# Optimization experiments

Hardware: AMD Instinct MI355X
Metric: run time of the kernel (lower is better)

## Reference

```python
import jax, jax.numpy as jnp
import numpy as np
import jax.scipy.linalg

BATCH = 1048576
M_NUM = 2
DT = 0.0166667
NN_RATIO = 0.5
SLOPE = 0.01  # torch LeakyReLU default negative_slope


def setup_inputs() -> dict:
    key = jax.random.key(0)
    ks = jax.random.split(key, 16)
    inp = {}
    inp["SS"] = jax.random.normal(ks[0], (BATCH, 2), dtype=jnp.float32)
    inp["Alphas"] = jax.random.uniform(ks[1], (BATCH, M_NUM), dtype=jnp.float32)
    # per-muscle scalar parameters (positive so sqrt(K*I) is valid)
    inp["K0s"] = jax.random.uniform(ks[2], (M_NUM,), minval=0.5, maxval=1.5)
    inp["K1s"] = jax.random.uniform(ks[3], (M_NUM,), minval=0.5, maxval=1.5)
    inp["L0s"] = jax.random.uniform(ks[4], (M_NUM,), minval=0.5, maxval=1.5)
    inp["L1s"] = jax.random.uniform(ks[5], (M_NUM,), minval=0.1, maxval=0.6)
    inp["Ms"] = jnp.array([1.0, -1.0], dtype=jnp.float32)  # moment arms
    inp["I_p"] = jnp.array([1.0], dtype=jnp.float32)
    inp["B_p"] = jnp.array([0.05], dtype=jnp.float32)
    inp["K_p"] = jnp.array([1.0], dtype=jnp.float32)
    # per-muscle compensational MLP weights: 3-32-32-32-1 (eval mode, dropout off)
    s = 0.1
    inp["W1"] = jax.random.normal(ks[6], (M_NUM, 3, 32)) * s
    inp["b1"] = jax.random.normal(ks[7], (M_NUM, 32)) * s
    inp["W2"] = jax.random.normal(ks[8], (M_NUM, 32, 32)) * s
    inp["b2"] = jax.random.normal(ks[9], (M_NUM, 32)) * s
    inp["W3"] = jax.random.normal(ks[10], (M_NUM, 32, 32)) * s
    inp["b3"] = jax.random.normal(ks[11], (M_NUM, 32)) * s
    inp["W4"] = jax.random.normal(ks[12], (M_NUM, 32, 1)) * s
    inp["b4"] = jax.random.normal(ks[13], (M_NUM, 1)) * s
    return inp


def _leaky(x):
    return jnp.where(x >= 0, x, SLOPE * x)


def reference(SS, Alphas, K0s, K1s, L0s, L1s, Ms, I_p, B_p, K_p,
              W1, b1, W2, b2, W3, b3, W4, b4):
    B = SS.shape[0]
    a = jnp.clip(Alphas, 0.0, 1.0)                      # (B, m)
    # muscle length / speed via scalar moment arms
    l = SS[:, 0:1] * Ms[None, :]                        # (B, m)
    dl = SS[:, 1:2] * Ms[None, :]                       # (B, m)
    # compensational MLPs, vectorized over muscles
    x = jnp.stack([l, dl, a], axis=-1)                  # (B, m, 3)
    h = _leaky(jnp.einsum('bmi,mio->bmo', x, W1) + b1[None])
    h = _leaky(jnp.einsum('bmi,mio->bmo', h, W2) + b2[None])
    h = _leaky(jnp.einsum('bmi,mio->bmo', h, W3) + b3[None])
    nn_out = jnp.tanh(jnp.einsum('bmi,mio->bmo', h, W4) + b4[None])[..., 0] * NN_RATIO  # (B, m)

    I0, B0p, K0p = I_p[0], B_p[0], K_p[0]
    K_m = K0s[None, :] + K1s[None, :] * a               # (B, m)
    K_tot = jnp.sum(K_m * Ms[None, :] ** 2, axis=1)     # (B,)
    A10 = -(K_tot + K0p) / I0
    D = 2.0 * jnp.sqrt(K_tot * I0)
    A11 = -(D + B0p) / I0
    B_F = K_m * (L0s[None, :] + L1s[None, :] * a - jnp.abs(l)) \
        + K1s[None, :] * L1s[None, :] * a * a * nn_out   # (B, m)
    B10 = jnp.sum(B_F * Ms[None, :], axis=1) / I0       # (B,)

    # Build block matrix M6 = [[A*dt, B*dt, 0], [0, 0, I2], [0, 0, 0]]
    M6 = jnp.zeros((B, 6, 6), dtype=SS.dtype)
    M6 = M6.at[:, 0, 1].set(DT)
    M6 = M6.at[:, 1, 0].set(A10 * DT)
    M6 = M6.at[:, 1, 1].set(A11 * DT)
    M6 = M6.at[:, 1, 2].set(B10 * DT)
    M6 = M6.at[:, 1, 3].set(DT / I0)
    M6 = M6.at[:, 2, 4].set(1.0)
    M6 = M6.at[:, 3, 5].set(1.0)

    expMT = jax.vmap(jax.scipy.linalg.expm)(M6)         # (B, 6, 6)
    Ad = expMT[:, :2, :2]
    Bd1 = expMT[:, :2, 4:6]
    Bd0 = expMT[:, :2, 2:4] - Bd1
    u = jnp.array([1.0, 0.0], dtype=SS.dtype)           # U0 = U1 = [1, 0]
    SSout = (jnp.einsum('bij,bj->bi', Ad, SS)
             + jnp.einsum('bij,j->bi', Bd0, u)
             + jnp.einsum('bij,j->bi', Bd1, u))          # (B, 2)
    return SSout[:, :1], SSout
```

## Files before the change

kernel.cpp:

```cpp
#include <hip/hip_runtime.h>
#include <hip/hip_bf16.h>

#define NTHREADS 256
#define WAVES    4
#define GPW      4
#define DT_F     0.0166667f

typedef _Float16 f16x4 __attribute__((ext_vector_type(4)));
typedef _Float16 f16x2 __attribute__((ext_vector_type(2)));
typedef float    f32x4 __attribute__((ext_vector_type(4)));

#define BF16_PROBE 0xBF803F80u

#define OW1 0
#define OB1 192
#define OW2 256
#define OB2 2304
#define OW3 2368
#define OB3 4416
#define OW4 4480
#define OB4 4544
#define SMEM_F 4560

__device__ __forceinline__ float leaky(float x) { return fmaxf(x, 0.01f * x); }

__device__ __forceinline__ float tanh_fast(float x) {
    const float xc = fminf(fmaxf(x, -10.0f), 10.0f);
    const float t  = __expf(2.0f * xc);
    return (t - 1.0f) * __builtin_amdgcn_rcpf(t + 1.0f);
}

__device__ __forceinline__ f16x2 pkrtz(float a, float b) {
    return __builtin_bit_cast(f16x2, __builtin_amdgcn_cvt_pkrtz(a, b));
}

__device__ __forceinline__ f16x4 leaky_cvt(const f32x4 D) {
    f16x2 lo = pkrtz(D[0], D[1]);
    f16x2 hi = pkrtz(D[2], D[3]);
    const f16x2 sl = {(_Float16)0.01f, (_Float16)0.01f};
    lo = __builtin_elementwise_max(lo, lo * sl);
    hi = __builtin_elementwise_max(hi, hi * sl);
    return __builtin_shufflevector(lo, hi, 0, 1, 2, 3);
}

__device__ __forceinline__ void epilogue_math(
    const float* P, float ss0, float ss1, float a0, float a1,
    float nn0, float nn1, float& o0f, float& o1f)
{
    const float K00 = P[0], K01 = P[1], K10 = P[2], K11 = P[3];
    const float L00 = P[4], L01 = P[5], L10 = P[6], L11 = P[7];
    const float Ms0 = P[8], Ms1 = P[9];
    const float I0  = P[10], B0p = P[11], K0p = P[12];

    const float Km0   = fmaf(K10, a0, K00);
    const float Km1   = fmaf(K11, a1, K01);
    const float K_tot = Km0*Ms0*Ms0 + Km1*Ms1*Ms1;
    const float invI  = 1.0f / I0;
    const float A10   = -(K_tot + K0p) * invI;
    const float Dd    = 2.0f * sqrtf(K_tot * I0);
    const float A11   = -(Dd + B0p) * invI;
    const float absl0 = fabsf(ss0 * Ms0);
    const float absl1 = fabsf(ss0 * Ms1);
    const float BF0   = Km0 * (L00 + L10*a0 - absl0) + K10*L10*a0*a0*nn0;
    const float BF1   = Km1 * (L01 + L11*a1 - absl1) + K11*L11*a1*a1*nn1;
    const float B10   = (BF0*Ms0 + BF1*Ms1) * invI;

    const float t01 = DT_F;
    const float t10 = A10 * DT_F;
    const float t11 = A11 * DT_F;

    float p00 = 1.0f/5040.0f, p01 = 0.0f, p10 = 0.0f, p11 = 1.0f/5040.0f;
    const float coef[6] = {1.0f/720.0f, 1.0f/120.0f, 1.0f/24.0f,
                           1.0f/6.0f,   0.5f,        1.0f};
    #pragma unroll
    for (int j = 0; j < 6; ++j) {
        const float cj  = coef[j];
        const float n00 = p01*t10 + cj;
        const float n01 = p00*t01 + p01*t11;
        const float n10 = p11*t10;
        const float n11 = p10*t01 + p11*t11 + cj;
        p00 = n00; p01 = n01; p10 = n10; p11 = n11;
    }
    const float e00 = 1.0f + t01*p10;
    const float e01 = t01*p11;
    const float e10 = t10*p00 + t11*p10;
    const float e11 = 1.0f + t10*p01 + t11*p11;

    const float cscale = DT_F * B10;
    o0f = fmaf(e00, ss0, fmaf(e01, ss1, p01 * cscale));
    o1f = fmaf(e10, ss0, fmaf(e11, ss1, p11 * cscale));
}

__device__ __forceinline__ float ldb(const __hip_bfloat16* p, int i) {
    return __bfloat162float(p[i]);
}

__device__ void run_bf16_fallback(
    const void* SSv, const void* ALv, const void* K0sv, const void* K1sv,
    const void* L0sv, const void* L1sv, const void* Msv, const void* I_pv,
    const void* B_pv, const void* K_pv, const void* W1v, const void* b1v,
    const void* W2v, const void* b2v, const void* W3v, const void* b3v,
    const void* W4v, const void* b4v, void* outv, int batch)
{
    const __hip_bfloat16* SS = (const __hip_bfloat16*)SSv;
    const __hip_bfloat16* AL = (const __hip_bfloat16*)ALv;
    const __hip_bfloat16* W1 = (const __hip_bfloat16*)W1v;
    const __hip_bfloat16* b1 = (const __hip_bfloat16*)b1v;
    const __hip_bfloat16* W2 = (const __hip_bfloat16*)W2v;
    const __hip_bfloat16* b2 = (const __hip_bfloat16*)b2v;
    const __hip_bfloat16* W3 = (const __hip_bfloat16*)W3v;
    const __hip_bfloat16* b3 = (const __hip_bfloat16*)b3v;
    const __hip_bfloat16* W4 = (const __hip_bfloat16*)W4v;
    const __hip_bfloat16* b4 = (const __hip_bfloat16*)b4v;

    float P[13];
    P[0] = ldb((const __hip_bfloat16*)K0sv, 0); P[1] = ldb((const __hip_bfloat16*)K0sv, 1);
    P[2] = ldb((const __hip_bfloat16*)K1sv, 0); P[3] = ldb((const __hip_bfloat16*)K1sv, 1);
    P[4] = ldb((const __hip_bfloat16*)L0sv, 0); P[5] = ldb((const __hip_bfloat16*)L0sv, 1);
    P[6] = ldb((const __hip_bfloat16*)L1sv, 0); P[7] = ldb((const __hip_bfloat16*)L1sv, 1);
    P[8] = ldb((const __hip_bfloat16*)Msv, 0);  P[9] = ldb((const __hip_bfloat16*)Msv, 1);
    P[10] = ldb((const __hip_bfloat16*)I_pv, 0);
    P[11] = ldb((const __hip_bfloat16*)B_pv, 0);
    P[12] = ldb((const __hip_bfloat16*)K_pv, 0);

    const int stride = gridDim.x * blockDim.x;
    for (int e = blockIdx.x * blockDim.x + threadIdx.x; e < batch; e += stride) {
        const float ss0 = ldb(SS, 2*e), ss1 = ldb(SS, 2*e+1);
        float a0 = fminf(fmaxf(ldb(AL, 2*e),   0.0f), 1.0f);
        float a1 = fminf(fmaxf(ldb(AL, 2*e+1), 0.0f), 1.0f);
        float nn[2];
        #pragma unroll 1
        for (int m = 0; m < 2; ++m) {
            const float am = m ? a1 : a0;
            const float l = ss0 * P[8+m], dl = ss1 * P[8+m];
            float h[32];
            #pragma unroll
            for (int o = 0; o < 32; ++o)
                h[o] = leaky(fmaf(l, ldb(W1, m*96+o),
                             fmaf(dl, ldb(W1, m*96+32+o),
                             fmaf(am, ldb(W1, m*96+64+o), ldb(b1, m*32+o)))));
            float g[32];
            #pragma unroll 1
            for (int oc = 0; oc < 4; ++oc) {
                float acc[8];
                #pragma unroll
                for (int j = 0; j < 8; ++j) acc[j] = ldb(b2, m*32+oc*8+j);
                #pragma unroll
                for (int k = 0; k < 32; ++k) {
                    #pragma unroll
                    for (int j = 0; j < 8; ++j)
                        acc[j] = fmaf(h[k], ldb(W2, m*1024+k*32+oc*8+j), acc[j]);
                }
                #pragma unroll
                for (int j = 0; j < 8; ++j) g[oc*8+j] = leaky(acc[j]);
            }
            float h3[32];
            #pragma unroll 1
            for (int oc = 0; oc < 4; ++oc) {
                float acc[8];
                #pragma unroll
                for (int j = 0; j < 8; ++j) acc[j] = ldb(b3, m*32+oc*8+j);
                #pragma unroll
                for (int k = 0; k < 32; ++k) {
                    #pragma unroll
                    for (int j = 0; j < 8; ++j)
                        acc[j] = fmaf(g[k], ldb(W3, m*1024+k*32+oc*8+j), acc[j]);
                }
                #pragma unroll
                for (int j = 0; j < 8; ++j) h3[oc*8+j] = leaky(acc[j]);
            }
            float acc = ldb(b4, m);
            #pragma unroll
            for (int k = 0; k < 32; ++k) acc = fmaf(h3[k], ldb(W4, m*32+k), acc);
            nn[m] = tanh_fast(acc) * 0.5f;
        }
        float o0f, o1f;
        epilogue_math(P, ss0, ss1, a0, a1, nn[0], nn[1], o0f, o1f);
        __hip_bfloat16* out0 = (__hip_bfloat16*)outv;
        __hip_bfloat162* out1 = (__hip_bfloat162*)(out0 + batch);
        out0[e] = __float2bfloat16(o0f);
        __hip_bfloat162 pr;
        pr.x = __float2bfloat16(o0f);
        pr.y = __float2bfloat16(o1f);
        out1[e] = pr;
    }
}

__global__ __launch_bounds__(NTHREADS) void joint_kernel(
    const void* __restrict__ SSv, const void* __restrict__ ALv,
    const void* __restrict__ K0sv, const void* __restrict__ K1sv,
    const void* __restrict__ L0sv, const void* __restrict__ L1sv,
    const void* __restrict__ Msv,  const void* __restrict__ I_pv,
    const void* __restrict__ B_pv, const void* __restrict__ K_pv,
    const void* __restrict__ W1v,  const void* __restrict__ b1v,
    const void* __restrict__ W2v,  const void* __restrict__ b2v,
    const void* __restrict__ W3v,  const void* __restrict__ b3v,
    const void* __restrict__ W4v,  const void* __restrict__ b4v,
    void* __restrict__ outv, int batch)
{
    const unsigned probe = *(const unsigned*)Msv;
    if (probe == BF16_PROBE) {
        run_bf16_fallback(SSv, ALv, K0sv, K1sv, L0sv, L1sv, Msv, I_pv, B_pv,
                          K_pv, W1v, b1v, W2v, b2v, W3v, b3v, W4v, b4v,
                          outv, batch);
        return;
    }

    const float* SS = (const float*)SSv;
    const float* AL = (const float*)ALv;
    const float* W1 = (const float*)W1v;  const float* b1 = (const float*)b1v;
    const float* W2 = (const float*)W2v;  const float* b2 = (const float*)b2v;
    const float* W3 = (const float*)W3v;  const float* b3 = (const float*)b3v;
    const float* W4 = (const float*)W4v;  const float* b4 = (const float*)b4v;

    const int tid  = threadIdx.x;
    const int wave = tid >> 6;
    const int lane = tid & 63;
    const int n    = lane & 15;
    const int q    = lane >> 4;

    __shared__ __align__(16) float sm[SMEM_F];
    for (int i = tid; i < 192;  i += NTHREADS) sm[OW1+i] = W1[i];
    for (int i = tid; i < 2048; i += NTHREADS) { sm[OW2+i] = W2[i]; sm[OW3+i] = W3[i]; }
    for (int i = tid; i < 64;   i += NTHREADS) {
        sm[OB1+i] = b1[i]; sm[OB2+i] = b2[i];
        sm[OB3+i] = b3[i]; sm[OW4+i] = W4[i];
    }
    if (tid < 2) sm[OB4+tid] = b4[tid];
    __syncthreads();

    f16x4 A1[2][2];
    #pragma unroll
    for (int mi = 0; mi < 2; ++mi)
        #pragma unroll
        for (int i = 0; i < 2; ++i)
            #pragma unroll
            for (int j = 0; j < 4; ++j) {
                const int k = q*4 + j;
                float v = 0.0f;
                if (k < 3)       v = sm[OW1 + mi*96 + k*32 + i*16 + n];
                else if (k == 3) v = sm[OB1 + mi*32 + i*16 + n];
                A1[mi][i][j] = (_Float16)v;
            }
    f16x4 A2[2][2][2], A3[2][2][2];
    #pragma unroll
    for (int mi = 0; mi < 2; ++mi)
        #pragma unroll
        for (int i = 0; i < 2; ++i)
            #pragma unroll
            for (int kb = 0; kb < 2; ++kb)
                #pragma unroll
                for (int j = 0; j < 4; ++j) {
                    const int in = kb*16 + q*4 + j;
                    A2[mi][i][kb][j] = (_Float16)sm[OW2 + mi*1024 + in*32 + i*16 + n];
                    A3[mi][i][kb][j] = (_Float16)sm[OW3 + mi*1024 + in*32 + i*16 + n];
                }
    f16x4 A4[2][2];
    #pragma unroll
    for (int mi = 0; mi < 2; ++mi)
        #pragma unroll
        for (int kb = 0; kb < 2; ++kb)
            #pragma unroll
            for (int j = 0; j < 4; ++j)
                A4[mi][kb][j] = (_Float16)sm[OW4 + mi*32 + kb*16 + q*4 + j];
    f32x4 Cb2[2][2], Cb3[2][2];
    #pragma unroll
    for (int mi = 0; mi < 2; ++mi) {
        #pragma unroll
        for (int i = 0; i < 2; ++i) {
            Cb2[mi][i] = *(const f32x4*)&sm[OB2 + mi*32 + i*16 + q*4];
            Cb3[mi][i] = *(const f32x4*)&sm[OB3 + mi*32 + i*16 + q*4];
        }
    }
    const float b4s0 = sm[OB4], b4s1 = sm[OB4+1];

    float P[13];
    P[0]  = ((const float*)K0sv)[0]; P[1]  = ((const float*)K0sv)[1];
    P[2]  = ((const float*)K1sv)[0]; P[3]  = ((const float*)K1sv)[1];
    P[4]  = ((const float*)L0sv)[0]; P[5]  = ((const float*)L0sv)[1];
    P[6]  = ((const float*)L1sv)[0]; P[7]  = ((const float*)L1sv)[1];
    P[8]  = ((const float*)Msv)[0];  P[9]  = ((const float*)Msv)[1];
    P[10] = ((const float*)I_pv)[0];
    P[11] = ((const float*)B_pv)[0];
    P[12] = ((const float*)K_pv)[0];

    const f32x4 zero = {0.0f, 0.0f, 0.0f, 0.0f};
    const int groupBase = (blockIdx.x * WAVES + wave) * GPW;

    #pragma unroll 1
    for (int g = 0; g < GPW; ++g) {
        const int ebase = (groupBase + g) * 64;
        float my_r0 = 0.0f, my_r1 = 0.0f;

        #pragma unroll 1
        for (int p = 0; p < 2; ++p) {
            const int t0 = 2*p, t1 = 2*p + 1;

            float2 s[2], al[2];
            float a0c[2], a1c[2];
            #pragma unroll
            for (int ti = 0; ti < 2; ++ti) {
                const int e  = ebase + (2*p + ti)*16 + n;
                const int eg = min(e, batch - 1);
                s[ti]  = ((const float2*)SS)[eg];
                al[ti] = ((const float2*)AL)[eg];
                a0c[ti] = fminf(fmaxf(al[ti].x, 0.0f), 1.0f);
                a1c[ti] = fminf(fmaxf(al[ti].y, 0.0f), 1.0f);
            }

            f16x4 B1[2][2];
            #pragma unroll
            for (int ti = 0; ti < 2; ++ti)
                #pragma unroll
                for (int mi = 0; mi < 2; ++mi) {
                    const float Msm = P[8 + mi];
                    const float am  = mi ? a1c[ti] : a0c[ti];
                    const f16x2 blo = pkrtz(s[ti].x * Msm, s[ti].y * Msm);
                    const f16x2 bhi = pkrtz(am, 1.0f);
                    B1[ti][mi] = __builtin_shufflevector(blo, bhi, 0, 1, 2, 3);
                }

            f32x4 D[2][2][2];
            #pragma unroll
            for (int ti = 0; ti < 2; ++ti)
                #pragma unroll
                for (int mi = 0; mi < 2; ++mi) {
                    D[ti][mi][0] = __builtin_amdgcn_mfma_f32_16x16x16f16(A1[mi][0], B1[ti][mi], zero, 0, 0, 0);
                    D[ti][mi][1] = __builtin_amdgcn_mfma_f32_16x16x16f16(A1[mi][1], B1[ti][mi], zero, 0, 0, 0);
                }
            f16x4 Bx[2][2][2];
            #pragma unroll
            for (int ti = 0; ti < 2; ++ti)
                #pragma unroll
                for (int mi = 0; mi < 2; ++mi) {
                    Bx[ti][mi][0] = leaky_cvt(D[ti][mi][0]);
                    Bx[ti][mi][1] = leaky_cvt(D[ti][mi][1]);
                }

            #pragma unroll
            for (int ti = 0; ti < 2; ++ti)
                #pragma unroll
                for (int mi = 0; mi < 2; ++mi) {
                    D[ti][mi][0] = __builtin_amdgcn_mfma_f32_16x16x16f16(A2[mi][0][1], Bx[ti][mi][1],
                                   __builtin_amdgcn_mfma_f32_16x16x16f16(A2[mi][0][0], Bx[ti][mi][0],
                                       Cb2[mi][0], 0, 0, 0), 0, 0, 0);
                    D[ti][mi][1] = __builtin_amdgcn_mfma_f32_16x16x16f16(A2[mi][1][1], Bx[ti][mi][1],
                                   __builtin_amdgcn_mfma_f32_16x16x16f16(A2[mi][1][0], Bx[ti][mi][0],
                                       Cb2[mi][1], 0, 0, 0), 0, 0, 0);
                }
            #pragma unroll
            for (int ti = 0; ti < 2; ++ti)
                #pragma unroll
                for (int mi = 0; mi < 2; ++mi) {
                    Bx[ti][mi][0] = leaky_cvt(D[ti][mi][0]);
                    Bx[ti][mi][1] = leaky_cvt(D[ti][mi][1]);
                }

            #pragma unroll
            for (int ti = 0; ti < 2; ++ti)
                #pragma unroll
                for (int mi = 0; mi < 2; ++mi) {
                    D[ti][mi][0] = __builtin_amdgcn_mfma_f32_16x16x16f16(A3[mi][0][1], Bx[ti][mi][1],
                                   __builtin_amdgcn_mfma_f32_16x16x16f16(A3[mi][0][0], Bx[ti][mi][0],
                                       Cb3[mi][0], 0, 0, 0), 0, 0, 0);
                    D[ti][mi][1] = __builtin_amdgcn_mfma_f32_16x16x16f16(A3[mi][1][1], Bx[ti][mi][1],
                                   __builtin_amdgcn_mfma_f32_16x16x16f16(A3[mi][1][0], Bx[ti][mi][0],
                                       Cb3[mi][1], 0, 0, 0), 0, 0, 0);
                }
            #pragma unroll
            for (int ti = 0; ti < 2; ++ti)
                #pragma unroll
                for (int mi = 0; mi < 2; ++mi) {
                    Bx[ti][mi][0] = leaky_cvt(D[ti][mi][0]);
                    Bx[ti][mi][1] = leaky_cvt(D[ti][mi][1]);
                }

            #pragma unroll
            for (int ti = 0; ti < 2; ++ti) {
                const bool own = (q == (2*p + ti));
                #pragma unroll
                for (int mi = 0; mi < 2; ++mi) {
                    f32x4 G = __builtin_amdgcn_mfma_f32_16x16x16f16(A4[mi][1], Bx[ti][mi][1],
                              __builtin_amdgcn_mfma_f32_16x16x16f16(A4[mi][0], Bx[ti][mi][0],
                                  zero, 0, 0, 0), 0, 0, 0);
                    const float r = G[0] + (mi ? b4s1 : b4s0);
                    if (mi == 0) my_r0 = own ? r : my_r0;
                    else         my_r1 = own ? r : my_r1;
                }
            }
        }

        const int eo  = ebase + lane;
        const int eog = min(eo, batch - 1);
        const float2 se  = ((const float2*)SS)[eog];
        const float2 ale = ((const float2*)AL)[eog];
        const float a0 = fminf(fmaxf(ale.x, 0.0f), 1.0f);
        const float a1 = fminf(fmaxf(ale.y, 0.0f), 1.0f);
        const float nn0 = tanh_fast(my_r0) * 0.5f;
        const float nn1 = tanh_fast(my_r1) * 0.5f;
        float o0f, o1f;
        epilogue_math(P, se.x, se.y, a0, a1, nn0, nn1, o0f, o1f);
        if (eo < batch) {
            ((float*)outv)[eo] = o0f;
            ((float2*)((float*)outv + batch))[eo] = make_float2(o0f, o1f);
        }
    }
}

extern "C" void kernel_launch(void* const* d_in, const int* in_sizes, int n_in,
                              void* d_out, int out_size, void* d_ws, size_t ws_size,
                              hipStream_t stream) {
    const int batch = in_sizes[0] / 2;
    const int elemsPerBlock = 64 * GPW * WAVES;
    const int grid = (batch + elemsPerBlock - 1) / elemsPerBlock;
    joint_kernel<<<grid, NTHREADS, 0, stream>>>(
        d_in[0], d_in[1], d_in[2], d_in[3], d_in[4], d_in[5], d_in[6],
        d_in[7], d_in[8], d_in[9], d_in[10], d_in[11], d_in[12], d_in[13],
        d_in[14], d_in[15], d_in[16], d_in[17], d_out, batch);
}
```

Baseline: 129.2 us.

## Use persistent grid-stride waves, pad weight LDS rows, shorten expm Taylor series

```diff
diff --git a/kernel.cpp b/kernel.cpp
--- a/kernel.cpp
+++ b/kernel.cpp
@@ -1,9 +1,9 @@
 #include <hip/hip_runtime.h>
 #include <hip/hip_bf16.h>
 
-#define NTHREADS 256
-#define WAVES    4
-#define GPW      4
+#define NTHREADS 512
+#define WAVES    8
+#define NBLOCKS  768
 #define DT_F     0.0166667f
 
 typedef _Float16 f16x4 __attribute__((ext_vector_type(4)));
@@ -15,12 +15,12 @@
 #define OW1 0
 #define OB1 192
 #define OW2 256
-#define OB2 2304
-#define OW3 2368
-#define OB3 4416
-#define OW4 4480
-#define OB4 4544
-#define SMEM_F 4560
+#define OB2 2368
+#define OW3 2432
+#define OB3 4544
+#define OW4 4608
+#define OB4 4672
+#define SMEM_F 4680
 
 __device__ __forceinline__ float leaky(float x) { return fmaxf(x, 0.01f * x); }
 
@@ -69,11 +69,10 @@
     const float t10 = A10 * DT_F;
     const float t11 = A11 * DT_F;
 
-    float p00 = 1.0f/5040.0f, p01 = 0.0f, p10 = 0.0f, p11 = 1.0f/5040.0f;
-    const float coef[6] = {1.0f/720.0f, 1.0f/120.0f, 1.0f/24.0f,
-                           1.0f/6.0f,   0.5f,        1.0f};
+    float p00 = 1.0f/120.0f, p01 = 0.0f, p10 = 0.0f, p11 = 1.0f/120.0f;
+    const float coef[4] = {1.0f/24.0f, 1.0f/6.0f, 0.5f, 1.0f};
     #pragma unroll
-    for (int j = 0; j < 6; ++j) {
+    for (int j = 0; j < 4; ++j) {
         const float cj  = coef[j];
         const float n00 = p01*t10 + cj;
         const float n01 = p00*t01 + p01*t11;
@@ -221,7 +220,11 @@
 
     __shared__ __align__(16) float sm[SMEM_F];
     for (int i = tid; i < 192;  i += NTHREADS) sm[OW1+i] = W1[i];
-    for (int i = tid; i < 2048; i += NTHREADS) { sm[OW2+i] = W2[i]; sm[OW3+i] = W3[i]; }
+    for (int i = tid; i < 2048; i += NTHREADS) {
+        const int mi = i >> 10, rem = i & 1023, in = rem >> 5, out = rem & 31;
+        sm[OW2 + mi*1056 + in*33 + out] = W2[i];
+        sm[OW3 + mi*1056 + in*33 + out] = W3[i];
+    }
     for (int i = tid; i < 64;   i += NTHREADS) {
         sm[OB1+i] = b1[i]; sm[OB2+i] = b2[i];
         sm[OB3+i] = b3[i]; sm[OW4+i] = W4[i];
@@ -252,8 +255,8 @@
                 #pragma unroll
                 for (int j = 0; j < 4; ++j) {
                     const int in = kb*16 + q*4 + j;
-                    A2[mi][i][kb][j] = (_Float16)sm[OW2 + mi*1024 + in*32 + i*16 + n];
-                    A3[mi][i][kb][j] = (_Float16)sm[OW3 + mi*1024 + in*32 + i*16 + n];
+                    A2[mi][i][kb][j] = (_Float16)sm[OW2 + mi*1056 + in*33 + i*16 + n];
+                    A3[mi][i][kb][j] = (_Float16)sm[OW3 + mi*1056 + in*33 + i*16 + n];
                 }
     f16x4 A4[2][2];
     #pragma unroll
@@ -285,27 +288,27 @@
     P[12] = ((const float*)K_pv)[0];
 
     const f32x4 zero = {0.0f, 0.0f, 0.0f, 0.0f};
-    const int groupBase = (blockIdx.x * WAVES + wave) * GPW;
+    const int nGroups    = (batch + 63) >> 6;
+    const int waveId     = blockIdx.x * WAVES + wave;
+    const int waveStride = gridDim.x * WAVES;
 
     #pragma unroll 1
-    for (int g = 0; g < GPW; ++g) {
-        const int ebase = (groupBase + g) * 64;
+    for (int grp = waveId; grp < nGroups; grp += waveStride) {
+        const int ebase = grp * 64;
         float my_r0 = 0.0f, my_r1 = 0.0f;
 
         #pragma unroll 1
         for (int p = 0; p < 2; ++p) {
-            const int t0 = 2*p, t1 = 2*p + 1;
-
-            float2 s[2], al[2];
+            float2 s[2];
             float a0c[2], a1c[2];
             #pragma unroll
             for (int ti = 0; ti < 2; ++ti) {
                 const int e  = ebase + (2*p + ti)*16 + n;
                 const int eg = min(e, batch - 1);
-                s[ti]  = ((const float2*)SS)[eg];
-                al[ti] = ((const float2*)AL)[eg];
-                a0c[ti] = fminf(fmaxf(al[ti].x, 0.0f), 1.0f);
-                a1c[ti] = fminf(fmaxf(al[ti].y, 0.0f), 1.0f);
+                s[ti] = ((const float2*)SS)[eg];
+                const float2 al = ((const float2*)AL)[eg];
+                a0c[ti] = fminf(fmaxf(al.x, 0.0f), 1.0f);
+                a1c[ti] = fminf(fmaxf(al.y, 0.0f), 1.0f);
             }
 
             f16x4 B1[2][2];
@@ -411,8 +414,10 @@
                               void* d_out, int out_size, void* d_ws, size_t ws_size,
                               hipStream_t stream) {
     const int batch = in_sizes[0] / 2;
-    const int elemsPerBlock = 64 * GPW * WAVES;
-    const int grid = (batch + elemsPerBlock - 1) / elemsPerBlock;
+    const int nGroups = (batch + 63) >> 6;
+    int grid = NBLOCKS;
+    const int maxBlocks = (nGroups + WAVES - 1) / WAVES;
+    if (grid > maxBlocks) grid = maxBlocks;
     joint_kernel<<<grid, NTHREADS, 0, stream>>>(
         d_in[0], d_in[1], d_in[2], d_in[3], d_in[4], d_in[5], d_in[6],
         d_in[7], d_in[8], d_in[9], d_in[10], d_in[11], d_in[12], d_in[13],
```

Result: no change. 129.0 us (-0.2%).
